# Performance work log

Hardware: AMD Instinct MI355X
Metric: run time of the kernel (lower is better)

The kernel has to match this reference:

```python
import jax, jax.numpy as jnp
import numpy as np

N = 50000          # num nodes
E = 800000         # num edges
H, C = 2, 64       # heads, per-head channels (hidden_dim=64)
IN_DIM = 128
EDGE_DIM = 32
NEG_SLOPE = 0.2


def setup_inputs() -> dict:
    key = jax.random.key(0)
    ks = jax.random.split(key, 20)
    s = 0.05
    inp = {
        'x': jax.random.normal(ks[0], (N, IN_DIM), jnp.float32),
        'edge_index': jax.random.randint(ks[1], (2, E), 0, N, jnp.int64),
        'edge_attr': jax.random.normal(ks[2], (E, EDGE_DIM), jnp.float32),
    }
    k = 3
    for l in range(3):
        inp[f'Wl{l}'] = jax.random.normal(ks[k], (IN_DIM, H * C), jnp.float32) * s; k += 1
        inp[f'Wr{l}'] = jax.random.normal(ks[k], (IN_DIM, H * C), jnp.float32) * s; k += 1
        inp[f'We{l}'] = jax.random.normal(ks[k], (EDGE_DIM, H * C), jnp.float32) * s; k += 1
        inp[f'att{l}'] = jax.random.normal(ks[k], (H, C), jnp.float32) * s; k += 1
        inp[f'b{l}'] = jnp.zeros((H * C,), jnp.float32)
    return inp


def gatv2_layer(x, src, dst, edge_attr, Wl, Wr, We, att, b):
    # PyG GATv2Conv (concat=True, share_weights=False):
    #   e_ij = att . LeakyReLU(Wl x_j + Wr x_i + We edge_ij)
    #   alpha = softmax_j over neighborhood of dst i; out_i = sum_j alpha_ij * (Wl x_j)
    xl = (x @ Wl).reshape(-1, H, C)              # [N,H,C] source transform
    xr = (x @ Wr).reshape(-1, H, C)              # [N,H,C] target transform
    ea = (edge_attr @ We).reshape(-1, H, C)      # [E,H,C]
    xj = xl[src]                                 # [E,H,C] gather source
    e = jax.nn.leaky_relu(xj + xr[dst] + ea, NEG_SLOPE)
    logits = jnp.einsum('ehc,hc->eh', e, att)    # [E,H]
    # segment softmax over dst neighborhoods
    m = jax.ops.segment_max(logits, dst, num_segments=N)  # [N,H]
    m = jnp.where(jnp.isfinite(m), m, 0.0)
    ex = jnp.exp(logits - m[dst])
    denom = jax.ops.segment_sum(ex, dst, num_segments=N)  # [N,H]
    alpha = ex / (denom[dst] + 1e-16)            # [E,H]
    out = jax.ops.segment_sum(alpha[:, :, None] * xj, dst, num_segments=N)  # [N,H,C]
    return out.reshape(-1, H * C) + b


def reference(x, edge_index, edge_attr,
              Wl0, Wr0, We0, att0, b0,
              Wl1, Wr1, We1, att1, b1,
              Wl2, Wr2, We2, att2, b2):
    src, dst = edge_index[0], edge_index[1]
    h = gatv2_layer(x, src, dst, edge_attr, Wl0, Wr0, We0, att0, b0)
    h = jax.nn.relu(h)
    h = gatv2_layer(h, src, dst, edge_attr, Wl1, Wr1, We1, att1, b1)
    h = jax.nn.relu(h)
    h = gatv2_layer(h, src, dst, edge_attr, Wl2, Wr2, We2, att2, b2)
    return h
```

## Files before the change

### kernel.cpp

```cpp
#include <hip/hip_runtime.h>

typedef unsigned int u32;
typedef unsigned short u16;
typedef __attribute__((ext_vector_type(8))) short bf16x8;
typedef __attribute__((ext_vector_type(4))) float f32x4;

__device__ __forceinline__ u16 f2b(float f){
  u32 x = __float_as_uint(f);
  u32 r = (x + 0x7fffu + ((x >> 16) & 1u)) >> 16;
  return (u16)r;
}
__device__ __forceinline__ float b2f(u16 h){ return __uint_as_float((u32)h << 16); }
__device__ __forceinline__ float bl(u32 u){ return __uint_as_float(u << 16); }
__device__ __forceinline__ float bh(u32 u){ return __uint_as_float(u & 0xffff0000u); }


__global__ void k_detect(const u32* __restrict__ ei, int n, u32* __restrict__ flag){
  int t = blockIdx.x * blockDim.x + threadIdx.x;
  u32 v = 0;
  if (t < n) v = ei[2 * t + 1];
  unsigned long long b = __ballot(v != 0u);
  if ((threadIdx.x & 63) == 0 && b) atomicOr(flag, 1u);
}

__global__ void k_convhist(const int* __restrict__ ei, int* __restrict__ src, int* __restrict__ dst,
                           int* __restrict__ deg, const float* __restrict__ eattr,
                           u16* __restrict__ ea2, int E, const u32* __restrict__ flag){
  int e = blockIdx.x * blockDim.x + threadIdx.x;
  if (e >= E) return;
  bool is64 = (*flag == 0u);
  int s, d;
  if (is64){ s = ei[2 * e]; d = ei[2 * (E + e)]; }
  else     { s = ei[e];     d = ei[E + e]; }
  src[e] = s; dst[e] = d;
  atomicAdd(&deg[d], 1);
  const float4* srow = (const float4*)(eattr + (size_t)e * 32);
  u32 pk[16];
  #pragma unroll
  for (int i = 0; i < 8; i++){
    float4 v = srow[i];
    pk[2*i]   = (u32)f2b(v.x) | ((u32)f2b(v.y) << 16);
    pk[2*i+1] = (u32)f2b(v.z) | ((u32)f2b(v.w) << 16);
  }
  uint4* drow = (uint4*)(ea2 + (size_t)e * 32);
  drow[0] = make_uint4(pk[0], pk[1], pk[2], pk[3]);
  drow[1] = make_uint4(pk[4], pk[5], pk[6], pk[7]);
  drow[2] = make_uint4(pk[8], pk[9], pk[10], pk[11]);
  drow[3] = make_uint4(pk[12], pk[13], pk[14], pk[15]);
}

__global__ __launch_bounds__(256) void k_scan1(const int* __restrict__ deg, int* __restrict__ bsum, int n,
                                               int* __restrict__ ssrc, int* __restrict__ sdst,
                                               u16* __restrict__ ea2s_pad, int E){
  int b = blockIdx.x, t = threadIdx.x, lane = t & 63, wv = t >> 6;
  if (b == 0){
    if (t < 64){ ssrc[E + t] = 0; sdst[E + t] = 0; }
    ((uint4*)ea2s_pad)[t] = make_uint4(0, 0, 0, 0);
  }
  int i0 = b * 1024 + t * 4;
  int4 v = make_int4(0,0,0,0);
  if (i0 + 3 < n) v = *(const int4*)(deg + i0);
  else { if (i0 < n) v.x = deg[i0]; if (i0+1 < n) v.y = deg[i0+1]; if (i0+2 < n) v.z = deg[i0+2]; }
  int s = v.x + v.y + v.z + v.w;
  #pragma unroll
  for (int off = 1; off < 64; off <<= 1) s += __shfl_xor(s, off);
  __shared__ int ws[4];
  if (lane == 0) ws[wv] = s;
  __syncthreads();
  if (t == 0) bsum[b] = ws[0] + ws[1] + ws[2] + ws[3];
}

__global__ __launch_bounds__(1024) void k_scan2(int* __restrict__ bsum, int nb, int* __restrict__ segN){
  int t = threadIdx.x, lane = t & 63, w = t >> 6;
  int v = (t < nb) ? bsum[t] : 0;
  int x = v;
  #pragma unroll
  for (int off = 1; off < 64; off <<= 1){
    int y = __shfl_up(x, off);
    if (lane >= off) x += y;
  }
  __shared__ int wsum[16];
  if (lane == 63) wsum[w] = x;
  __syncthreads();
  if (w == 0 && lane < 16){
    int sv = wsum[lane];
    #pragma unroll
    for (int off = 1; off < 16; off <<= 1){
      int y = __shfl_up(sv, off);
      if (lane >= off) sv += y;
    }
    wsum[lane] = sv;
  }
  __syncthreads();
  int woff = (w > 0) ? wsum[w - 1] : 0;
  if (t < nb) bsum[t] = woff + x - v;
  if (t == 0) *segN = wsum[15];
}

__global__ __launch_bounds__(256) void k_scan3(const int* __restrict__ deg, const int* __restrict__ bsum,
                                               int* __restrict__ seg, int n){
  int b = blockIdx.x, t = threadIdx.x, lane = t & 63, wv = t >> 6;
  int i0 = b * 1024 + t * 4;
  int4 v = make_int4(0,0,0,0);
  if (i0 + 3 < n) v = *(const int4*)(deg + i0);
  else { if (i0 < n) v.x = deg[i0]; if (i0+1 < n) v.y = deg[i0+1]; if (i0+2 < n) v.z = deg[i0+2]; }
  int s = v.x + v.y + v.z + v.w;
  int x = s;
  #pragma unroll
  for (int off = 1; off < 64; off <<= 1){
    int y = __shfl_up(x, off);
    if (lane >= off) x += y;
  }
  __shared__ int ws[4];
  if (lane == 63) ws[wv] = x;
  __syncthreads();
  int woff = 0;
  #pragma unroll
  for (int k = 0; k < 4; k++) if (k < wv) woff += ws[k];
  int base = bsum[b] + woff + (x - s);
  if (i0 < n)     seg[i0]     = base;
  if (i0+1 < n)   seg[i0+1]   = base + v.x;
  if (i0+2 < n)   seg[i0+2]   = base + v.x + v.y;
  if (i0+3 < n)   seg[i0+3]   = base + v.x + v.y + v.z;
}

__global__ void k_scatter(const int* __restrict__ src, const int* __restrict__ dst,
                          const int* __restrict__ seg, int* __restrict__ cur,
                          int* __restrict__ ssrc, int* __restrict__ sdst,
                          int* __restrict__ seid, int E){
  int e = blockIdx.x * blockDim.x + threadIdx.x;
  if (e >= E) return;
  int d = dst[e];
  int pos = seg[d] + atomicAdd(&cur[d], 1);
  ssrc[pos] = src[e];
  sdst[pos] = d;
  seid[pos] = e;
}

__global__ void k_sortb(const int* __restrict__ seid, const u16* __restrict__ ea2o,
                        u16* __restrict__ ea2s, int E){
  int t = blockIdx.x * blockDim.x + threadIdx.x;
  int e = t >> 2, j = t & 3;
  if (e >= E) return;
  int eid = seid[e];
  uint4 v = *(const uint4*)(ea2o + (size_t)eid * 32 + j * 8);
  *(uint4*)(ea2s + (size_t)e * 32 + j * 8) = v;
}

__global__ __launch_bounds__(256) void k_prepw(
    const float* __restrict__ W0, const float* __restrict__ W1, const float* __restrict__ W2,
    const float* __restrict__ W3, const float* __restrict__ W4, const float* __restrict__ W5,
    u16* __restrict__ WtH, u16* __restrict__ WtL)
{
  int mat = blockIdx.z;
  const float* W = (mat == 0) ? W0 : (mat == 1) ? W1 : (mat == 2) ? W2 :
                   (mat == 3) ? W3 : (mat == 4) ? W4 : W5;
  __shared__ float tile[32][33];
  int kt = blockIdx.x * 32, ct = blockIdx.y * 32;
  int tr = threadIdx.x & 31, ti = threadIdx.x >> 5;
  #pragma unroll
  for (int j = 0; j < 4; j++){
    int kk = ti + 8 * j;
    tile[kk][tr] = W[(size_t)(kt + kk) * 128 + ct + tr];
  }
  __syncthreads();
  #pragma unroll
  for (int j = 0; j < 4; j++){
    int cc = ti + 8 * j;
    float v = tile[tr][cc];
    u16 hi = f2b(v);
    u16 lo = f2b(v - b2f(hi));
    size_t o = (size_t)mat * 16384 + (size_t)(ct + cc) * 128 + kt + tr;
    WtH[o] = hi;
    WtL[o] = lo;
  }
}

__global__ __launch_bounds__(256) void k_gemm2(
    const float* __restrict__ A,
    const u16* __restrict__ WtH, const u16* __restrict__ WtL,
    u16* __restrict__ xlb, u16* __restrict__ xrb, int nrows)
{
  __shared__ u16 sAH[64][32], sAL[64][32];
  __shared__ u16 sWH[128][32], sWL[128][32];
  int t = threadIdx.x, wv = t >> 6, lane = t & 63;
  int col = lane & 15, kg = lane >> 4;
  int r0 = blockIdx.x * 64;
  int mat = blockIdx.y;
  const u16* WHb = WtH + (size_t)mat * 16384;
  const u16* WLb = WtL + (size_t)mat * 16384;

  f32x4 acc[4][2];
  #pragma unroll
  for (int m = 0; m < 4; m++)
    #pragma unroll
    for (int n = 0; n < 2; n++)
      acc[m][n] = (f32x4){0.f, 0.f, 0.f, 0.f};

  int ar = t >> 2, ak = (t & 3) << 3;
  int wc = t >> 1, wk = (t & 1) << 4;

  for (int kh = 0; kh < 4; kh++){
    __syncthreads();
    {
      int gr = r0 + ar;
      const float* ap = A + (size_t)gr * 128 + kh * 32 + ak;
      float4 va = {0,0,0,0}, vb = {0,0,0,0};
      if (gr < nrows){ va = *(const float4*)ap; vb = *(const float4*)(ap + 4); }
      float fv[8] = { va.x, va.y, va.z, va.w, vb.x, vb.y, vb.z, vb.w };
      u32 hp[4], lp[4];
      #pragma unroll
      for (int i = 0; i < 4; i++){
        u16 h0 = f2b(fv[2*i]),   h1 = f2b(fv[2*i+1]);
        u16 l0 = f2b(fv[2*i]   - b2f(h0));
        u16 l1 = f2b(fv[2*i+1] - b2f(h1));
        hp[i] = (u32)h0 | ((u32)h1 << 16);
        lp[i] = (u32)l0 | ((u32)l1 << 16);
      }
      *(uint4*)&sAH[ar][ak] = make_uint4(hp[0], hp[1], hp[2], hp[3]);
      *(uint4*)&sAL[ar][ak] = make_uint4(lp[0], lp[1], lp[2], lp[3]);
    }
    {
      const u16* gh = WHb + (size_t)wc * 128 + kh * 32 + wk;
      const u16* gl = WLb + (size_t)wc * 128 + kh * 32 + wk;
      uint4 h0 = *(const uint4*)gh, h1 = *(const uint4*)(gh + 8);
      uint4 l0 = *(const uint4*)gl, l1 = *(const uint4*)(gl + 8);
      *(uint4*)&sWH[wc][wk]     = h0; *(uint4*)&sWH[wc][wk + 8] = h1;
      *(uint4*)&sWL[wc][wk]     = l0; *(uint4*)&sWL[wc][wk + 8] = l1;
    }
    __syncthreads();
    bf16x8 bhi0 = *(const bf16x8*)&sWH[wv*32 + col]     [kg*8];
    bf16x8 bhi1 = *(const bf16x8*)&sWH[wv*32 + 16 + col][kg*8];
    bf16x8 blo0 = *(const bf16x8*)&sWL[wv*32 + col]     [kg*8];
    bf16x8 blo1 = *(const bf16x8*)&sWL[wv*32 + 16 + col][kg*8];
    #pragma unroll
    for (int m = 0; m < 4; m++){
      bf16x8 ahv = *(const bf16x8*)&sAH[m*16 + col][kg*8];
      bf16x8 alv = *(const bf16x8*)&sAL[m*16 + col][kg*8];
      acc[m][0] = __builtin_amdgcn_mfma_f32_16x16x32_bf16(ahv, bhi0, acc[m][0], 0, 0, 0);
      acc[m][0] = __builtin_amdgcn_mfma_f32_16x16x32_bf16(alv, bhi0, acc[m][0], 0, 0, 0);
      acc[m][0] = __builtin_amdgcn_mfma_f32_16x16x32_bf16(ahv, blo0, acc[m][0], 0, 0, 0);
      acc[m][1] = __builtin_amdgcn_mfma_f32_16x16x32_bf16(ahv, bhi1, acc[m][1], 0, 0, 0);
      acc[m][1] = __builtin_amdgcn_mfma_f32_16x16x32_bf16(alv, bhi1, acc[m][1], 0, 0, 0);
      acc[m][1] = __builtin_amdgcn_mfma_f32_16x16x32_bf16(ahv, blo1, acc[m][1], 0, 0, 0);
    }
  }
  u16* ob = mat ? xrb : xlb;
  #pragma unroll
  for (int m = 0; m < 4; m++){
    #pragma unroll
    for (int n = 0; n < 2; n++){
      #pragma unroll
      for (int r = 0; r < 4; r++){
        int row = r0 + m*16 + kg*4 + r;
        int c   = wv*32 + n*16 + col;
        if (row < nrows) ob[(size_t)row * 128 + c] = f2b(acc[m][n][r]);
      }
    }
  }
}

__global__ __launch_bounds__(256) void k_edge(
    const int* __restrict__ ssrc, const int* __restrict__ sdst,
    const u16* __restrict__ ea2s,
    const u16* __restrict__ xlb, const u16* __restrict__ xrb,
    const float* __restrict__ We, const float* __restrict__ att,
    float2* __restrict__ pr2, int ntiles, int E)
{
  __shared__ float sD[4][16][132];
  int wv = threadIdx.x >> 6, lane = threadIdx.x & 63;
  int col = lane & 15, kg = lane >> 4;
  int er = lane >> 2, q = lane & 3;

  bf16x8 bw[8];
  #pragma unroll
  for (int c = 0; c < 8; c++)
    #pragma unroll
    for (int j = 0; j < 8; j++)
      bw[c][j] = (short)f2b(We[(kg * 8 + j) * 128 + c * 16 + col]);
  u32 attp[16];
  #pragma unroll
  for (int i = 0; i < 16; i++)
    attp[i] = (u32)f2b(att[q * 32 + 2*i]) | ((u32)f2b(att[q * 32 + 2*i + 1]) << 16);

  int nw = gridDim.x * 4;
  int t = blockIdx.x * 4 + wv;
  if (t >= ntiles) return;

  int e0 = t * 16;
  bf16x8 a = *(const bf16x8*)(ea2s + (size_t)(e0 + col) * 32 + kg * 8);
  int p = e0 + er;
  int sn = ssrc[p], dn = sdst[p];
  const u16* xjp = xlb + (size_t)sn * 128 + q * 32;
  uint4 j0 = ((const uint4*)xjp)[0], j1 = ((const uint4*)xjp)[1],
        j2 = ((const uint4*)xjp)[2], j3 = ((const uint4*)xjp)[3];

  while (true){
    const u16* xip = xrb + (size_t)dn * 128 + q * 32;
    uint4 i0 = ((const uint4*)xip)[0], i1 = ((const uint4*)xip)[1],
          i2 = ((const uint4*)xip)[2], i3 = ((const uint4*)xip)[3];

    int t2 = t + nw;
    bool more = (t2 < ntiles);
    int tc = more ? t2 : t;
    int e02 = tc * 16;
    int p2 = e02 + er;
    int sn2 = ssrc[p2], dn2 = sdst[p2];
    bf16x8 a2 = *(const bf16x8*)(ea2s + (size_t)(e02 + col) * 32 + kg * 8);
    const u16* xj2 = xlb + (size_t)sn2 * 128 + q * 32;
    uint4 nj0 = ((const uint4*)xj2)[0], nj1 = ((const uint4*)xj2)[1],
          nj2 = ((const uint4*)xj2)[2], nj3 = ((const uint4*)xj2)[3];

    #pragma unroll
    for (int c = 0; c < 8; c++){
      f32x4 d = __builtin_amdgcn_mfma_f32_16x16x32_bf16(a, bw[c], (f32x4){0.f,0.f,0.f,0.f}, 0, 0, 0);
      #pragma unroll
      for (int r = 0; r < 4; r++)
        sD[wv][kg * 4 + r][c * 16 + col] = d[r];
    }

    const float* drow = &sD[wv][er][q * 32];
    float acc = 0.f;
#define EPK(KO, JQ, IQ) { \
    float4 d0 = *(const float4*)(drow + KO*8); \
    float4 d1 = *(const float4*)(drow + KO*8 + 4); \
    float v; u32 jw, iw, aw; \
    jw = JQ.x; iw = IQ.x; aw = attp[KO*4+0]; \
    v = d0.x + bl(jw) + bl(iw); v = fmaxf(v, 0.2f*v); acc = fmaf(v, bl(aw), acc); \
    v = d0.y + bh(jw) + bh(iw); v = fmaxf(v, 0.2f*v); acc = fmaf(v, bh(aw), acc); \
    jw = JQ.y; iw = IQ.y; aw = attp[KO*4+1]; \
    v = d0.z + bl(jw) + bl(iw); v = fmaxf(v, 0.2f*v); acc = fmaf(v, bl(aw), acc); \
    v = d0.w + bh(jw) + bh(iw); v = fmaxf(v, 0.2f*v); acc = fmaf(v, bh(aw), acc); \
    jw = JQ.z; iw = IQ.z; aw = attp[KO*4+2]; \
    v = d1.x + bl(jw) + bl(iw); v = fmaxf(v, 0.2f*v); acc = fmaf(v, bl(aw), acc); \
    v = d1.y + bh(jw) + bh(iw); v = fmaxf(v, 0.2f*v); acc = fmaf(v, bh(aw), acc); \
    jw = JQ.w; iw = IQ.w; aw = attp[KO*4+3]; \
    v = d1.z + bl(jw) + bl(iw); v = fmaxf(v, 0.2f*v); acc = fmaf(v, bl(aw), acc); \
    v = d1.w + bh(jw) + bh(iw); v = fmaxf(v, 0.2f*v); acc = fmaf(v, bh(aw), acc); }
    EPK(0, j0, i0) EPK(1, j1, i1) EPK(2, j2, i2) EPK(3, j3, i3)
#undef EPK
    acc += __shfl_xor(acc, 1);
    float other = __shfl_xor(acc, 2);
    if (q == 0 && p < E){
      pr2[p] = make_float2(__expf(fminf(acc, 80.f)), __expf(fminf(other, 80.f)));
    }
    if (!more) break;
    t = t2; p = p2; dn = dn2; a = a2;
    j0 = nj0; j1 = nj1; j2 = nj2; j3 = nj3;
  }
}

template<int RELU>
__global__ __launch_bounds__(256) void k_seg2(
    const int* __restrict__ seg, const int* __restrict__ ssrc,
    const float2* __restrict__ pr2,
    const u16* __restrict__ xlb, const float* __restrict__ bias,
    float* __restrict__ out, int N)
{
  int wid  = blockIdx.x * 4 + (threadIdx.x >> 6);
  int lane = threadIdx.x & 63;
  if (wid >= N) return;
  int eg = lane >> 4, cb = lane & 15, c0 = cb * 8;
  int hsel = cb >> 3;

  int p0 = seg[wid], p1 = seg[wid + 1];
  float s = 0.f;
  float o0 = 0.f, o1 = 0.f, o2 = 0.f, o3 = 0.f, o4 = 0.f, o5 = 0.f, o6 = 0.f, o7 = 0.f;

  if (p0 < p1){
#define LDB(PP, QV, XV) { \
    int ii = PP + eg; ii = (ii < p1) ? ii : (p1 - 1); \
    int sn = ssrc[ii]; \
    QV = pr2[ii]; \
    XV = *(const uint4*)(xlb + (size_t)sn * 128 + c0); }
    float2 qa; uint4 xa;
    LDB(p0, qa, xa)
    int p = p0;
    while (true){
      int pn = p + 4;
      bool more = pn < p1;
      int pc = more ? pn : p;
      float2 qb; uint4 xb;
      LDB(pc, qb, xb)
      float e = hsel ? qa.y : qa.x;
      if (p + eg >= p1) e = 0.f;
      s += e;
      o0 = fmaf(e, bl(xa.x), o0); o1 = fmaf(e, bh(xa.x), o1);
      o2 = fmaf(e, bl(xa.y), o2); o3 = fmaf(e, bh(xa.y), o3);
      o4 = fmaf(e, bl(xa.z), o4); o5 = fmaf(e, bh(xa.z), o5);
      o6 = fmaf(e, bl(xa.w), o6); o7 = fmaf(e, bh(xa.w), o7);
      if (!more) break;
      p = pn; qa = qb; xa = xb;
    }
#undef LDB
  }
  s  += __shfl_xor(s, 16);  s  += __shfl_xor(s, 32);
  o0 += __shfl_xor(o0, 16); o0 += __shfl_xor(o0, 32);
  o1 += __shfl_xor(o1, 16); o1 += __shfl_xor(o1, 32);
  o2 += __shfl_xor(o2, 16); o2 += __shfl_xor(o2, 32);
  o3 += __shfl_xor(o3, 16); o3 += __shfl_xor(o3, 32);
  o4 += __shfl_xor(o4, 16); o4 += __shfl_xor(o4, 32);
  o5 += __shfl_xor(o5, 16); o5 += __shfl_xor(o5, 32);
  o6 += __shfl_xor(o6, 16); o6 += __shfl_xor(o6, 32);
  o7 += __shfl_xor(o7, 16); o7 += __shfl_xor(o7, 32);

  if (eg == 0){
    float inv = 1.0f / (s + 1e-16f);
    float4 b0 = *(const float4*)(bias + c0);
    float4 b1 = *(const float4*)(bias + c0 + 4);
    float r0 = fmaf(o0, inv, b0.x), r1 = fmaf(o1, inv, b0.y);
    float r2 = fmaf(o2, inv, b0.z), r3 = fmaf(o3, inv, b0.w);
    float r4 = fmaf(o4, inv, b1.x), r5 = fmaf(o5, inv, b1.y);
    float r6 = fmaf(o6, inv, b1.z), r7 = fmaf(o7, inv, b1.w);
    if (RELU){
      r0 = fmaxf(r0, 0.f); r1 = fmaxf(r1, 0.f); r2 = fmaxf(r2, 0.f); r3 = fmaxf(r3, 0.f);
      r4 = fmaxf(r4, 0.f); r5 = fmaxf(r5, 0.f); r6 = fmaxf(r6, 0.f); r7 = fmaxf(r7, 0.f);
    }
    *(float4*)(out + (size_t)wid * 128 + c0)     = make_float4(r0, r1, r2, r3);
    *(float4*)(out + (size_t)wid * 128 + c0 + 4) = make_float4(r4, r5, r6, r7);
  }
}

extern "C" void kernel_launch(void* const* d_in, const int* in_sizes, int n_in,
                              void* d_out, int out_size, void* d_ws, size_t ws_size,
                              hipStream_t stream)
{
  const float* x     = (const float*)d_in[0];
  const int*   ei    = (const int*)  d_in[1];
  const float* eattr = (const float*)d_in[2];
  const float* Wp[3][5];
  for (int l = 0; l < 3; l++)
    for (int j = 0; j < 5; j++)
      Wp[l][j] = (const float*)d_in[3 + l * 5 + j];

  int N = in_sizes[0] / 128;
  int E = in_sizes[2] / 32;

  char* w = (char*)d_ws;
  auto alloc = [&](size_t bytes) -> char* {
    char* p = w; w += (bytes + 255) & ~(size_t)255; return p;
  };
  float* xr   = (float*)alloc((size_t)N * 128 * 4);
  u16*   xlb  = (u16*)  alloc((size_t)N * 128 * 2);
  u16*   xrb  = (u16*)  alloc((size_t)N * 128 * 2);
  u16*   ea2o = (u16*)  alloc((size_t)E * 32 * 2);
  u16*   ea2s = (u16*)  alloc((size_t)(E + 64) * 32 * 2);
  float2* prb = (float2*)alloc((size_t)E * 8);
  u16*   WtH  = (u16*)  alloc((size_t)6 * 16384 * 2);
  u16*   WtL  = (u16*)  alloc((size_t)6 * 16384 * 2);
  int* srcA   = (int*)alloc((size_t)E * 4);
  int* dstA   = (int*)alloc((size_t)E * 4);
  int* ssrc   = (int*)alloc((size_t)(E + 64) * 4);
  int* sdst   = (int*)alloc((size_t)(E + 64) * 4);
  int* seid   = (int*)alloc((size_t)E * 4);
  int* seg    = (int*)alloc((size_t)(N + 1) * 4);
  int* bsum   = (int*)alloc(1024 * 4);
  char* zbase = alloc((size_t)N * 4);      int* deg  = (int*)zbase;
  char* zcur  = alloc((size_t)N * 4);      int* cur  = (int*)zcur;
  char* zflag = alloc(256);                u32* flag = (u32*)zflag;
  size_t zspan = (size_t)(zflag + 256 - zbase);

  hipMemsetAsync(zbase, 0, zspan, stream);

  int ndet = (E < 16384) ? E : 16384;
  k_detect<<<(ndet + 255) / 256, 256, 0, stream>>>((const u32*)ei, ndet, flag);
  int gE = (E + 255) / 256;
  k_convhist<<<gE, 256, 0, stream>>>(ei, srcA, dstA, deg, eattr, ea2o, E, flag);
  int nb = (N + 1023) / 1024;
  k_scan1<<<nb, 256, 0, stream>>>(deg, bsum, N, ssrc, sdst, ea2s + (size_t)E * 32, E);
  k_scan2<<<1, 1024, 0, stream>>>(bsum, nb, seg + N);
  k_scan3<<<nb, 256, 0, stream>>>(deg, bsum, seg, N);
  k_scatter<<<gE, 256, 0, stream>>>(srcA, dstA, seg, cur, ssrc, sdst, seid, E);
  k_sortb<<<(E * 4 + 255) / 256, 256, 0, stream>>>(seid, ea2o, ea2s, E);
  dim3 gp(4, 4, 6);
  k_prepw<<<gp, 256, 0, stream>>>(Wp[0][0], Wp[0][1], Wp[1][0], Wp[1][1], Wp[2][0], Wp[2][1], WtH, WtL);

  int gS = (N + 3) / 4;
  int ntiles = (E + 15) / 16;
  int gEdge = (ntiles + 3) / 4; if (gEdge > 2048) gEdge = 2048;
  dim3 gG2((N + 63) / 64, 2);

  const float* hin = x;
  for (int l = 0; l < 3; l++){
    k_gemm2<<<gG2, 256, 0, stream>>>(hin, WtH + (size_t)l * 2 * 16384, WtL + (size_t)l * 2 * 16384, xlb, xrb, N);
    k_edge<<<gEdge, 256, 0, stream>>>(ssrc, sdst, ea2s, xlb, xrb, Wp[l][2], Wp[l][3], prb, ntiles, E);
    float* outp = (l == 2) ? (float*)d_out : xr;
    if (l == 2) k_seg2<0><<<gS, 256, 0, stream>>>(seg, ssrc, prb, xlb, Wp[l][4], outp, N);
    else        k_seg2<1><<<gS, 256, 0, stream>>>(seg, ssrc, prb, xlb, Wp[l][4], outp, N);
    hin = xr;
  }
}
```

Measured before the change: 478.9 us.

## Fuse edge-logit and segment-softmax aggregation into one node-centric kernel

Replaces the edge-parallel logit kernel and the per-node aggregation kernel with a single kernel that runs one wave per destination node. Each wave walks the node's CSR edge range in 16-edge MFMA tiles, computes exp-logits, and accumulates the weighted source features in registers. This drops the intermediate probability buffer, the sorted dst array and the second gather of source features. The costs are a per-wave reload of We and att, MFMA work wasted on partially filled tiles, loss of the cross-tile prefetch, and a heavier shuffle reduction over 32 accumulators per lane.

New measurement: 855.6 us. 1.79x slower.

```diff
diff --git a/kernel.cpp b/kernel.cpp
--- a/kernel.cpp
+++ b/kernel.cpp
@@ -49,14 +49,8 @@
   drow[3] = make_uint4(pk[12], pk[13], pk[14], pk[15]);
 }
 
-__global__ __launch_bounds__(256) void k_scan1(const int* __restrict__ deg, int* __restrict__ bsum, int n,
-                                               int* __restrict__ ssrc, int* __restrict__ sdst,
-                                               u16* __restrict__ ea2s_pad, int E){
+__global__ __launch_bounds__(256) void k_scan1(const int* __restrict__ deg, int* __restrict__ bsum, int n){
   int b = blockIdx.x, t = threadIdx.x, lane = t & 63, wv = t >> 6;
-  if (b == 0){
-    if (t < 64){ ssrc[E + t] = 0; sdst[E + t] = 0; }
-    ((uint4*)ea2s_pad)[t] = make_uint4(0, 0, 0, 0);
-  }
   int i0 = b * 1024 + t * 4;
   int4 v = make_int4(0,0,0,0);
   if (i0 + 3 < n) v = *(const int4*)(deg + i0);
@@ -126,14 +120,12 @@
 
 __global__ void k_scatter(const int* __restrict__ src, const int* __restrict__ dst,
                           const int* __restrict__ seg, int* __restrict__ cur,
-                          int* __restrict__ ssrc, int* __restrict__ sdst,
-                          int* __restrict__ seid, int E){
+                          int* __restrict__ ssrc, int* __restrict__ seid, int E){
   int e = blockIdx.x * blockDim.x + threadIdx.x;
   if (e >= E) return;
   int d = dst[e];
   int pos = seg[d] + atomicAdd(&cur[d], 1);
   ssrc[pos] = src[e];
-  sdst[pos] = d;
   seid[pos] = e;
 }
 
@@ -260,17 +252,34 @@
   }
 }
 
-__global__ __launch_bounds__(256) void k_edge(
-    const int* __restrict__ ssrc, const int* __restrict__ sdst,
+template<int RELU>
+__global__ __launch_bounds__(256) void k_node(
+    const int* __restrict__ seg, const int* __restrict__ ssrc,
     const u16* __restrict__ ea2s,
     const u16* __restrict__ xlb, const u16* __restrict__ xrb,
     const float* __restrict__ We, const float* __restrict__ att,
-    float2* __restrict__ pr2, int ntiles, int E)
+    const float* __restrict__ bias,
+    float* __restrict__ out, int N)
 {
   __shared__ float sD[4][16][132];
   int wv = threadIdx.x >> 6, lane = threadIdx.x & 63;
   int col = lane & 15, kg = lane >> 4;
   int er = lane >> 2, q = lane & 3;
+  int wid = blockIdx.x * 4 + wv;
+  if (wid >= N) return;
+
+  int p0 = seg[wid], p1 = seg[wid + 1];
+  if (p0 == p1){
+    if (er == 0){
+      #pragma unroll
+      for (int i = 0; i < 8; i++){
+        float4 b = *(const float4*)(bias + q * 32 + i * 4);
+        if (RELU){ b.x = fmaxf(b.x,0.f); b.y = fmaxf(b.y,0.f); b.z = fmaxf(b.z,0.f); b.w = fmaxf(b.w,0.f); }
+        *(float4*)(out + (size_t)wid * 128 + q * 32 + i * 4) = b;
+      }
+    }
+    return;
+  }
 
   bf16x8 bw[8];
   #pragma unroll
@@ -283,33 +292,25 @@
   for (int i = 0; i < 16; i++)
     attp[i] = (u32)f2b(att[q * 32 + 2*i]) | ((u32)f2b(att[q * 32 + 2*i + 1]) << 16);
 
-  int nw = gridDim.x * 4;
-  int t = blockIdx.x * 4 + wv;
-  if (t >= ntiles) return;
-
-  int e0 = t * 16;
-  bf16x8 a = *(const bf16x8*)(ea2s + (size_t)(e0 + col) * 32 + kg * 8);
-  int p = e0 + er;
-  int sn = ssrc[p], dn = sdst[p];
-  const u16* xjp = xlb + (size_t)sn * 128 + q * 32;
-  uint4 j0 = ((const uint4*)xjp)[0], j1 = ((const uint4*)xjp)[1],
-        j2 = ((const uint4*)xjp)[2], j3 = ((const uint4*)xjp)[3];
-
-  while (true){
-    const u16* xip = xrb + (size_t)dn * 128 + q * 32;
-    uint4 i0 = ((const uint4*)xip)[0], i1 = ((const uint4*)xip)[1],
-          i2 = ((const uint4*)xip)[2], i3 = ((const uint4*)xip)[3];
-
-    int t2 = t + nw;
-    bool more = (t2 < ntiles);
-    int tc = more ? t2 : t;
-    int e02 = tc * 16;
-    int p2 = e02 + er;
-    int sn2 = ssrc[p2], dn2 = sdst[p2];
-    bf16x8 a2 = *(const bf16x8*)(ea2s + (size_t)(e02 + col) * 32 + kg * 8);
-    const u16* xj2 = xlb + (size_t)sn2 * 128 + q * 32;
-    uint4 nj0 = ((const uint4*)xj2)[0], nj1 = ((const uint4*)xj2)[1],
-          nj2 = ((const uint4*)xj2)[2], nj3 = ((const uint4*)xj2)[3];
+  const u16* xir = xrb + (size_t)wid * 128 + q * 32;
+  uint4 i0 = ((const uint4*)xir)[0], i1 = ((const uint4*)xir)[1],
+        i2 = ((const uint4*)xir)[2], i3 = ((const uint4*)xir)[3];
+
+  float s = 0.f;
+  float oacc[32];
+  #pragma unroll
+  for (int i = 0; i < 32; i++) oacc[i] = 0.f;
+
+  for (int p = p0; p < p1; p += 16){
+    int ia = p + col; ia = (ia < p1) ? ia : (p1 - 1);
+    bf16x8 a = *(const bf16x8*)(ea2s + (size_t)ia * 32 + kg * 8);
+    int pe = p + er;
+    bool live = (pe < p1);
+    pe = live ? pe : (p1 - 1);
+    int sn = ssrc[pe];
+    const u16* xjr = xlb + (size_t)sn * 128 + q * 32;
+    uint4 j0 = ((const uint4*)xjr)[0], j1 = ((const uint4*)xjr)[1],
+          j2 = ((const uint4*)xjr)[2], j3 = ((const uint4*)xjr)[3];
 
     #pragma unroll
     for (int c = 0; c < 8; c++){
@@ -340,84 +341,44 @@
     EPK(0, j0, i0) EPK(1, j1, i1) EPK(2, j2, i2) EPK(3, j3, i3)
 #undef EPK
     acc += __shfl_xor(acc, 1);
-    float other = __shfl_xor(acc, 2);
-    if (q == 0 && p < E){
-      pr2[p] = make_float2(__expf(fminf(acc, 80.f)), __expf(fminf(other, 80.f)));
-    }
-    if (!more) break;
-    t = t2; p = p2; dn = dn2; a = a2;
-    j0 = nj0; j1 = nj1; j2 = nj2; j3 = nj3;
-  }
-}
-
-template<int RELU>
-__global__ __launch_bounds__(256) void k_seg2(
-    const int* __restrict__ seg, const int* __restrict__ ssrc,
-    const float2* __restrict__ pr2,
-    const u16* __restrict__ xlb, const float* __restrict__ bias,
-    float* __restrict__ out, int N)
-{
-  int wid  = blockIdx.x * 4 + (threadIdx.x >> 6);
-  int lane = threadIdx.x & 63;
-  if (wid >= N) return;
-  int eg = lane >> 4, cb = lane & 15, c0 = cb * 8;
-  int hsel = cb >> 3;
-
-  int p0 = seg[wid], p1 = seg[wid + 1];
-  float s = 0.f;
-  float o0 = 0.f, o1 = 0.f, o2 = 0.f, o3 = 0.f, o4 = 0.f, o5 = 0.f, o6 = 0.f, o7 = 0.f;
-
-  if (p0 < p1){
-#define LDB(PP, QV, XV) { \
-    int ii = PP + eg; ii = (ii < p1) ? ii : (p1 - 1); \
-    int sn = ssrc[ii]; \
-    QV = pr2[ii]; \
-    XV = *(const uint4*)(xlb + (size_t)sn * 128 + c0); }
-    float2 qa; uint4 xa;
-    LDB(p0, qa, xa)
-    int p = p0;
-    while (true){
-      int pn = p + 4;
-      bool more = pn < p1;
-      int pc = more ? pn : p;
-      float2 qb; uint4 xb;
-      LDB(pc, qb, xb)
-      float e = hsel ? qa.y : qa.x;
-      if (p + eg >= p1) e = 0.f;
-      s += e;
-      o0 = fmaf(e, bl(xa.x), o0); o1 = fmaf(e, bh(xa.x), o1);
-      o2 = fmaf(e, bl(xa.y), o2); o3 = fmaf(e, bh(xa.y), o3);
-      o4 = fmaf(e, bl(xa.z), o4); o5 = fmaf(e, bh(xa.z), o5);
-      o6 = fmaf(e, bl(xa.w), o6); o7 = fmaf(e, bh(xa.w), o7);
-      if (!more) break;
-      p = pn; qa = qb; xa = xb;
-    }
-#undef LDB
-  }
-  s  += __shfl_xor(s, 16);  s  += __shfl_xor(s, 32);
-  o0 += __shfl_xor(o0, 16); o0 += __shfl_xor(o0, 32);
-  o1 += __shfl_xor(o1, 16); o1 += __shfl_xor(o1, 32);
-  o2 += __shfl_xor(o2, 16); o2 += __shfl_xor(o2, 32);
-  o3 += __shfl_xor(o3, 16); o3 += __shfl_xor(o3, 32);
-  o4 += __shfl_xor(o4, 16); o4 += __shfl_xor(o4, 32);
-  o5 += __shfl_xor(o5, 16); o5 += __shfl_xor(o5, 32);
-  o6 += __shfl_xor(o6, 16); o6 += __shfl_xor(o6, 32);
-  o7 += __shfl_xor(o7, 16); o7 += __shfl_xor(o7, 32);
-
-  if (eg == 0){
+    float pr = __expf(fminf(acc, 80.f));
+    if (!live) pr = 0.f;
+    s += pr;
+#define OAC(KO, JQ) { \
+    oacc[KO*8+0] = fmaf(pr, bl(JQ.x), oacc[KO*8+0]); \
+    oacc[KO*8+1] = fmaf(pr, bh(JQ.x), oacc[KO*8+1]); \
+    oacc[KO*8+2] = fmaf(pr, bl(JQ.y), oacc[KO*8+2]); \
+    oacc[KO*8+3] = fmaf(pr, bh(JQ.y), oacc[KO*8+3]); \
+    oacc[KO*8+4] = fmaf(pr, bl(JQ.z), oacc[KO*8+4]); \
+    oacc[KO*8+5] = fmaf(pr, bh(JQ.z), oacc[KO*8+5]); \
+    oacc[KO*8+6] = fmaf(pr, bl(JQ.w), oacc[KO*8+6]); \
+    oacc[KO*8+7] = fmaf(pr, bh(JQ.w), oacc[KO*8+7]); }
+    OAC(0, j0) OAC(1, j1) OAC(2, j2) OAC(3, j3)
+#undef OAC
+  }
+
+  s += __shfl_xor(s, 4); s += __shfl_xor(s, 8); s += __shfl_xor(s, 16); s += __shfl_xor(s, 32);
+  #pragma unroll
+  for (int i = 0; i < 32; i++){
+    oacc[i] += __shfl_xor(oacc[i], 4);
+    oacc[i] += __shfl_xor(oacc[i], 8);
+    oacc[i] += __shfl_xor(oacc[i], 16);
+    oacc[i] += __shfl_xor(oacc[i], 32);
+  }
+
+  if (er == 0){
     float inv = 1.0f / (s + 1e-16f);
-    float4 b0 = *(const float4*)(bias + c0);
-    float4 b1 = *(const float4*)(bias + c0 + 4);
-    float r0 = fmaf(o0, inv, b0.x), r1 = fmaf(o1, inv, b0.y);
-    float r2 = fmaf(o2, inv, b0.z), r3 = fmaf(o3, inv, b0.w);
-    float r4 = fmaf(o4, inv, b1.x), r5 = fmaf(o5, inv, b1.y);
-    float r6 = fmaf(o6, inv, b1.z), r7 = fmaf(o7, inv, b1.w);
-    if (RELU){
-      r0 = fmaxf(r0, 0.f); r1 = fmaxf(r1, 0.f); r2 = fmaxf(r2, 0.f); r3 = fmaxf(r3, 0.f);
-      r4 = fmaxf(r4, 0.f); r5 = fmaxf(r5, 0.f); r6 = fmaxf(r6, 0.f); r7 = fmaxf(r7, 0.f);
-    }
-    *(float4*)(out + (size_t)wid * 128 + c0)     = make_float4(r0, r1, r2, r3);
-    *(float4*)(out + (size_t)wid * 128 + c0 + 4) = make_float4(r4, r5, r6, r7);
+    #pragma unroll
+    for (int i = 0; i < 8; i++){
+      float4 b = *(const float4*)(bias + q * 32 + i * 4);
+      float4 r;
+      r.x = fmaf(oacc[4*i],     inv, b.x);
+      r.y = fmaf(oacc[4*i + 1], inv, b.y);
+      r.z = fmaf(oacc[4*i + 2], inv, b.z);
+      r.w = fmaf(oacc[4*i + 3], inv, b.w);
+      if (RELU){ r.x = fmaxf(r.x,0.f); r.y = fmaxf(r.y,0.f); r.z = fmaxf(r.z,0.f); r.w = fmaxf(r.w,0.f); }
+      *(float4*)(out + (size_t)wid * 128 + q * 32 + i * 4) = r;
+    }
   }
 }
 
@@ -444,14 +405,12 @@
   u16*   xlb  = (u16*)  alloc((size_t)N * 128 * 2);
   u16*   xrb  = (u16*)  alloc((size_t)N * 128 * 2);
   u16*   ea2o = (u16*)  alloc((size_t)E * 32 * 2);
-  u16*   ea2s = (u16*)  alloc((size_t)(E + 64) * 32 * 2);
-  float2* prb = (float2*)alloc((size_t)E * 8);
+  u16*   ea2s = (u16*)  alloc((size_t)E * 32 * 2);
   u16*   WtH  = (u16*)  alloc((size_t)6 * 16384 * 2);
   u16*   WtL  = (u16*)  alloc((size_t)6 * 16384 * 2);
   int* srcA   = (int*)alloc((size_t)E * 4);
   int* dstA   = (int*)alloc((size_t)E * 4);
-  int* ssrc   = (int*)alloc((size_t)(E + 64) * 4);
-  int* sdst   = (int*)alloc((size_t)(E + 64) * 4);
+  int* ssrc   = (int*)alloc((size_t)E * 4);
   int* seid   = (int*)alloc((size_t)E * 4);
   int* seg    = (int*)alloc((size_t)(N + 1) * 4);
   int* bsum   = (int*)alloc(1024 * 4);
@@ -467,26 +426,23 @@
   int gE = (E + 255) / 256;
   k_convhist<<<gE, 256, 0, stream>>>(ei, srcA, dstA, deg, eattr, ea2o, E, flag);
   int nb = (N + 1023) / 1024;
-  k_scan1<<<nb, 256, 0, stream>>>(deg, bsum, N, ssrc, sdst, ea2s + (size_t)E * 32, E);
+  k_scan1<<<nb, 256, 0, stream>>>(deg, bsum, N);
   k_scan2<<<1, 1024, 0, stream>>>(bsum, nb, seg + N);
   k_scan3<<<nb, 256, 0, stream>>>(deg, bsum, seg, N);
-  k_scatter<<<gE, 256, 0, stream>>>(srcA, dstA, seg, cur, ssrc, sdst, seid, E);
+  k_scatter<<<gE, 256, 0, stream>>>(srcA, dstA, seg, cur, ssrc, seid, E);
   k_sortb<<<(E * 4 + 255) / 256, 256, 0, stream>>>(seid, ea2o, ea2s, E);
   dim3 gp(4, 4, 6);
   k_prepw<<<gp, 256, 0, stream>>>(Wp[0][0], Wp[0][1], Wp[1][0], Wp[1][1], Wp[2][0], Wp[2][1], WtH, WtL);
 
-  int gS = (N + 3) / 4;
-  int ntiles = (E + 15) / 16;
-  int gEdge = (ntiles + 3) / 4; if (gEdge > 2048) gEdge = 2048;
+  int gN = (N + 3) / 4;
   dim3 gG2((N + 63) / 64, 2);
 
   const float* hin = x;
   for (int l = 0; l < 3; l++){
     k_gemm2<<<gG2, 256, 0, stream>>>(hin, WtH + (size_t)l * 2 * 16384, WtL + (size_t)l * 2 * 16384, xlb, xrb, N);
-    k_edge<<<gEdge, 256, 0, stream>>>(ssrc, sdst, ea2s, xlb, xrb, Wp[l][2], Wp[l][3], prb, ntiles, E);
     float* outp = (l == 2) ? (float*)d_out : xr;
-    if (l == 2) k_seg2<0><<<gS, 256, 0, stream>>>(seg, ssrc, prb, xlb, Wp[l][4], outp, N);
-    else        k_seg2<1><<<gS, 256, 0, stream>>>(seg, ssrc, prb, xlb, Wp[l][4], outp, N);
+    if (l == 2) k_node<0><<<gN, 256, 0, stream>>>(seg, ssrc, ea2s, xlb, xrb, Wp[l][2], Wp[l][3], Wp[l][4], outp, N);
+    else        k_node<1><<<gN, 256, 0, stream>>>(seg, ssrc, ea2s, xlb, xrb, Wp[l][2], Wp[l][3], Wp[l][4], outp, N);
     hin = xr;
   }
 }
```
